# Kernel optimization log

Hardware: AMD Instinct MI355X
Metric: run time of the kernel (lower is better)

Reference implementation:

```python
import jax, jax.numpy as jnp
import numpy as np

HEADS = 12
EMBED = 768
HEAD_DIM = EMBED // HEADS


def setup_inputs() -> dict:
    key = jax.random.key(0)
    kx, kw, kb = jax.random.split(key, 3)
    x = jax.random.normal(kx, (8, 1024, EMBED), dtype=jnp.float32)
    # nn.Linear(embed, 3*embed): weight (3E, E), bias (3E,)
    W_qkv = jax.random.normal(kw, (3 * EMBED, EMBED), dtype=jnp.float32) * (1.0 / np.sqrt(EMBED))
    b_qkv = jax.random.normal(kb, (3 * EMBED,), dtype=jnp.float32) * 0.01
    return {"x": x, "W_qkv": W_qkv, "b_qkv": b_qkv}


def reference(x, W_qkv, b_qkv):
    b, n, e = x.shape
    qkv = x @ W_qkv.T + b_qkv                       # (b, n, 3E)
    qkv = qkv.reshape(b, n, HEADS, 3 * HEAD_DIM)    # (b, n, h, 3d)
    q, k, v = jnp.split(qkv, 3, axis=-1)            # each (b, n, h, d)
    scores = jnp.einsum('bihd,bjhd->bijh', q, k) / np.sqrt(HEAD_DIM)
    attn = jax.nn.softmax(scores, axis=-2)          # softmax over keys j (dim=-2)
    out = jnp.einsum('bijh,bjhd->bihd', attn, v)
    return out.reshape(b, n, e)
```

## Files before the change

kernel.cpp:

```cpp
#include <hip/hip_runtime.h>
#include <hip/hip_bf16.h>
#include <cstdint>
#include <math.h>

#define BATCH 8
#define SEQ   1024
#define EMB   768
#define HEADS 12
#define HDIM  64
#define C3    2304
#define MROWS (BATCH*SEQ)
#define NKT   (EMB / 32)
#define MTILES (MROWS / 128)
#define NTILES (C3 / 128)
#define XPACK_BLOCKS (MTILES * NKT)
#define WPACK_BLOCKS (NTILES * NKT)

typedef __attribute__((ext_vector_type(8)))  short bf16x8;
typedef __attribute__((ext_vector_type(4)))  short bf16x4;
typedef __attribute__((ext_vector_type(4)))  float f32x4;

static __device__ inline short f2bf(float f) {
    union { float f; uint32_t u; } v; v.f = f;
    uint32_t u = v.u + 0x7fff + ((v.u >> 16) & 1);
    return (short)(u >> 16);
}

static __device__ __forceinline__ void gload_lds16(const short* g, short* l) {
    __builtin_amdgcn_global_load_lds(
        (const __attribute__((address_space(1))) unsigned int*)g,
        (__attribute__((address_space(3))) unsigned int*)l, 16, 0, 0);
}

__global__ __launch_bounds__(256) void pack_bf16(const float* __restrict__ x,
                                                 short* __restrict__ xb2,
                                                 const float* __restrict__ W,
                                                 short* __restrict__ Wb2) {
    const float* in;
    short* out;
    int blk;
    if (blockIdx.x < XPACK_BLOCKS) {
        in = x; out = xb2; blk = blockIdx.x;
    } else {
        in = W; out = Wb2; blk = blockIdx.x - XPACK_BLOCKS;
    }
    const int mt = blk / NKT;
    const int kt = blk % NKT;
    short* obase = out + (size_t)blk * 4096;

    #pragma unroll
    for (int p = 0; p < 2; ++p) {
        int idx = p * 256 + threadIdx.x;
        int r = idx >> 2, s = idx & 3;
        const float* src = in + (size_t)(mt * 128 + r) * EMB + kt * 32 + s * 8;
        float4 v0 = ((const float4*)src)[0];
        float4 v1 = ((const float4*)src)[1];
        bf16x8 o = { f2bf(v0.x), f2bf(v0.y), f2bf(v0.z), f2bf(v0.w),
                     f2bf(v1.x), f2bf(v1.y), f2bf(v1.z), f2bf(v1.w) };
        int S = ((4 * r + s) ^ (r & 7));
        *(bf16x8*)(obase + S * 8) = o;
    }
}

#define LVP 136

__global__ __launch_bounds__(256) void qkv_gemm_mfma(const short* __restrict__ Apk,
                                                     const short* __restrict__ Bpk,
                                                     const float* __restrict__ bias,
                                                     short* __restrict__ qkvb,
                                                     short* __restrict__ vt) {
    __shared__ short smem[16384];
    short (*As)[4096] = (short (*)[4096])smem;
    short (*Bs)[4096] = (short (*)[4096])(smem + 8192);
    short* Lv = smem;

    const int g    = blockIdx.x;
    const int xcd  = g & 7;
    const int ring = g >> 3;
    const int by   = xcd * 8 + (ring & 7);
    const int bx   = ring >> 3;

    const int t    = threadIdx.x;
    const int w    = t >> 6;
    const int lane = t & 63;
    const int s4   = lane >> 4;
    const int r15  = lane & 15;
    const int m0 = by * 128, n0 = bx * 128;
    const int wm = (w & 1) * 64, wn = (w >> 1) * 64;

    const short* Ab = Apk + (size_t)by * (NKT * 4096);
    const short* Bb = Bpk + (size_t)bx * (NKT * 4096);

    int offA[4], offB[4];
    #pragma unroll
    for (int i = 0; i < 4; ++i) {
        int ra = wm + i * 16 + r15;
        offA[i] = ((4 * ra + s4) ^ (ra & 7)) << 3;
        int rb = wn + i * 16 + r15;
        offB[i] = ((4 * rb + s4) ^ (rb & 7)) << 3;
    }

    const int seg0 = w * 2;

#define STAGE(buf, kt) do {                                                   \
        const short* _a = Ab + (size_t)(kt) * 4096;                           \
        const short* _b = Bb + (size_t)(kt) * 4096;                           \
        gload_lds16(_a + (seg0    ) * 512 + lane * 8, &As[buf][(seg0    ) * 512]); \
        gload_lds16(_b + (seg0    ) * 512 + lane * 8, &Bs[buf][(seg0    ) * 512]); \
        gload_lds16(_a + (seg0 + 1) * 512 + lane * 8, &As[buf][(seg0 + 1) * 512]); \
        gload_lds16(_b + (seg0 + 1) * 512 + lane * 8, &Bs[buf][(seg0 + 1) * 512]); \
    } while (0)

    f32x4 acc[4][4] = {};

#define COMPUTE(buf) do {                                                     \
        bf16x8 af[4], bff[4];                                                 \
        _Pragma("unroll")                                                     \
        for (int i = 0; i < 4; ++i) {                                         \
            af[i]  = *(const bf16x8*)&As[buf][offA[i]];                       \
            bff[i] = *(const bf16x8*)&Bs[buf][offB[i]];                       \
        }                                                                     \
        _Pragma("unroll")                                                     \
        for (int mi = 0; mi < 4; ++mi)                                        \
            _Pragma("unroll")                                                 \
            for (int ni = 0; ni < 4; ++ni)                                    \
                acc[mi][ni] = __builtin_amdgcn_mfma_f32_16x16x32_bf16(        \
                    af[mi], bff[ni], acc[mi][ni], 0, 0, 0);                   \
    } while (0)

    STAGE(0, 0);
    __syncthreads();

    for (int kt = 0; kt < NKT; kt += 2) {
        STAGE(1, kt + 1);
        COMPUTE(0);
        __syncthreads();
        if (kt + 2 < NKT) STAGE(0, kt + 2);
        COMPUTE(1);
        __syncthreads();
    }
#undef STAGE
#undef COMPUTE

    const int bxm   = bx % 3;
    const bool has_v    = (bxm != 0);
    const int  wn_v     = (bxm == 1) ? 0 : 64;
    const bool is_vwave = has_v && (wn == wn_v);

    float bsv[4], scl[4];
    #pragma unroll
    for (int ni = 0; ni < 4; ++ni) {
        int n = n0 + wn + ni * 16 + r15;
        bsv[ni] = bias[n];
        scl[ni] = ((n % 192) < 64) ? 0.125f : 1.0f;
    }

    if (!is_vwave) {
        #pragma unroll
        for (int mi = 0; mi < 4; ++mi) {
            const int m = m0 + wm + mi * 16 + s4 * 4;
            #pragma unroll
            for (int ni = 0; ni < 4; ++ni) {
                const int n = n0 + wn + ni * 16 + r15;
                #pragma unroll
                for (int reg = 0; reg < 4; ++reg)
                    qkvb[(size_t)(m + reg) * C3 + n] =
                        f2bf((acc[mi][ni][reg] + bsv[ni]) * scl[ni]);
            }
        }
    } else {
        #pragma unroll
        for (int mi = 0; mi < 4; ++mi) {
            const int jl = wm + mi * 16 + s4 * 4;
            #pragma unroll
            for (int ni = 0; ni < 4; ++ni) {
                const int d = ni * 16 + r15;
                bf16x4 vv = { f2bf(acc[mi][ni][0] + bsv[ni]),
                              f2bf(acc[mi][ni][1] + bsv[ni]),
                              f2bf(acc[mi][ni][2] + bsv[ni]),
                              f2bf(acc[mi][ni][3] + bsv[ni]) };
                *(bf16x4*)&Lv[d * LVP + jl] = vv;
            }
        }
    }

    if (has_v) {
        __syncthreads();
        const int h  = (n0 + wn_v) / 192;
        const int bb = by >> 3;
        const int j0 = m0 & 1023;
        short* vrow = vt + ((size_t)(bb * HEADS + h) * 64) * SEQ + j0;
        #pragma unroll
        for (int p = 0; p < 4; ++p) {
            int lin = p * 256 + t;
            int d   = lin >> 4;
            int ch  = lin & 15;
            *(bf16x8*)(vrow + (size_t)d * SEQ + ch * 8) =
                *(bf16x8*)&Lv[d * LVP + ch * 8];
        }
    }
}

__global__ __launch_bounds__(256, 4) void attn_mfma(const short* __restrict__ qkvb,
                                                    const short* __restrict__ vt,
                                                    float* __restrict__ out) {
    __shared__ short Ks[64][64];
    __shared__ short Vt[64][64];
    __shared__ short Ps[64][64];

    const int g    = blockIdx.x;
    const int qt   = g / (BATCH * HEADS);
    const int bh   = g % (BATCH * HEADS);
    const int b    = bh / HEADS;
    const int h    = bh % HEADS;
    const int t    = threadIdx.x;
    const int w    = t >> 6;
    const int lane = t & 63;
    const int c    = lane & 15;
    const int q    = lane >> 4;
    const int ck   = c & 7;
    const int i0   = qt * 64;

    const size_t base = (size_t)b * SEQ * C3 + (size_t)h * 192;
    const short* vtb = vt + (size_t)bh * 64 * SEQ;
    const short* gk  = qkvb + base + 64;

    bf16x8 aq0, aq1;
    {
        const short* pq = qkvb + base + (size_t)(i0 + w * 16 + c) * C3 + q * 8;
        aq0 = *(const bf16x8*)(pq);
        aq1 = *(const bf16x8*)(pq + 32);
    }

    const int jA = t >> 3;
    const int jB = jA + 32;
    const int sg = t & 7;
    const int wKA = (sg ^ (jA & 7)) * 8;
    const int wKB = (sg ^ (jB & 7)) * 8;

    bf16x8 kr0, kr1, vr0, vr1;
    kr0 = *(const bf16x8*)(gk + (size_t)jA * C3 + sg * 8);
    kr1 = *(const bf16x8*)(gk + (size_t)jB * C3 + sg * 8);
    vr0 = *(const bf16x8*)(vtb + (size_t)jA * SEQ + sg * 8);
    vr1 = *(const bf16x8*)(vtb + (size_t)jB * SEQ + sg * 8);

    f32x4 o[4] = {};
    float l_acc = 0.f;

    for (int kt = 0; kt < 16; ++kt) {
        __syncthreads();
        *(bf16x8*)&Ks[jA][wKA] = kr0;
        *(bf16x8*)&Ks[jB][wKB] = kr1;
        *(bf16x8*)&Vt[jA][wKA] = vr0;
        *(bf16x8*)&Vt[jB][wKB] = vr1;
        __syncthreads();

        if (kt < 15) {
            const int j0 = (kt + 1) * 64;
            kr0 = *(const bf16x8*)(gk + (size_t)(j0 + jA) * C3 + sg * 8);
            kr1 = *(const bf16x8*)(gk + (size_t)(j0 + jB) * C3 + sg * 8);
            vr0 = *(const bf16x8*)(vtb + (size_t)jA * SEQ + j0 + sg * 8);
            vr1 = *(const bf16x8*)(vtb + (size_t)jB * SEQ + j0 + sg * 8);
        }

        bf16x8 ka[4][2];
        #pragma unroll
        for (int mt = 0; mt < 4; ++mt) {
            ka[mt][0] = *(bf16x8*)&Ks[mt * 16 + c][(q ^ ck) * 8];
            ka[mt][1] = *(bf16x8*)&Ks[mt * 16 + c][((4 + q) ^ ck) * 8];
        }

        f32x4 s[4];
        __builtin_amdgcn_s_setprio(1);
        #pragma unroll
        for (int mt = 0; mt < 4; ++mt) {
            f32x4 acc = {0.f, 0.f, 0.f, 0.f};
            acc = __builtin_amdgcn_mfma_f32_16x16x32_bf16(ka[mt][0], aq0, acc, 0, 0, 0);
            acc = __builtin_amdgcn_mfma_f32_16x16x32_bf16(ka[mt][1], aq1, acc, 0, 0, 0);
            s[mt] = acc;
        }
        __builtin_amdgcn_s_setprio(0);

        #pragma unroll
        for (int mt = 0; mt < 4; ++mt) {
            float p0 = __expf(s[mt][0]);
            float p1 = __expf(s[mt][1]);
            float p2 = __expf(s[mt][2]);
            float p3 = __expf(s[mt][3]);
            l_acc += (p0 + p1) + (p2 + p3);
            bf16x4 pw = { f2bf(p0), f2bf(p1), f2bf(p2), f2bf(p3) };
            int pcol = (((2 * mt + (q >> 1)) ^ ck) << 3) + (q & 1) * 4;
            *(bf16x4*)&Ps[w * 16 + c][pcol] = pw;
        }

        bf16x8 vb[4][2];
        #pragma unroll
        for (int dt = 0; dt < 4; ++dt) {
            vb[dt][0] = *(bf16x8*)&Vt[dt * 16 + c][(q ^ ck) * 8];
            vb[dt][1] = *(bf16x8*)&Vt[dt * 16 + c][((4 + q) ^ ck) * 8];
        }

        bf16x8 ap0 = *(bf16x8*)&Ps[w * 16 + c][(q ^ ck) * 8];
        bf16x8 ap1 = *(bf16x8*)&Ps[w * 16 + c][((4 + q) ^ ck) * 8];
        __builtin_amdgcn_s_setprio(1);
        #pragma unroll
        for (int dt = 0; dt < 4; ++dt) {
            o[dt] = __builtin_amdgcn_mfma_f32_16x16x32_bf16(ap0, vb[dt][0], o[dt], 0, 0, 0);
            o[dt] = __builtin_amdgcn_mfma_f32_16x16x32_bf16(ap1, vb[dt][1], o[dt], 0, 0, 0);
        }
        __builtin_amdgcn_s_setprio(0);
    }

    float v = l_acc;
    v += __shfl_xor(v, 16, 64);
    v += __shfl_xor(v, 32, 64);
    float linv[4];
    #pragma unroll
    for (int r = 0; r < 4; ++r)
        linv[r] = 1.0f / __shfl(v, 4 * q + r, 64);

    #pragma unroll
    for (int dt = 0; dt < 4; ++dt)
        #pragma unroll
        for (int r = 0; r < 4; ++r) {
            int i = w * 16 + q * 4 + r;
            out[((size_t)b * SEQ + i0 + i) * EMB + h * HDIM + dt * 16 + c]
                = o[dt][r] * linv[r];
        }
}

extern "C" void kernel_launch(void* const* d_in, const int* in_sizes, int n_in,
                              void* d_out, int out_size, void* d_ws, size_t ws_size,
                              hipStream_t stream) {
    const float* x    = (const float*)d_in[0];
    const float* W    = (const float*)d_in[1];
    const float* bias = (const float*)d_in[2];
    float* out = (float*)d_out;

    short* xb2  = (short*)d_ws;
    short* Wb2  = xb2 + (size_t)MROWS * EMB;
    short* qkvb = Wb2 + (size_t)C3 * EMB;
    short* vt   = qkvb + (size_t)MROWS * C3;

    pack_bf16<<<XPACK_BLOCKS + WPACK_BLOCKS, 256, 0, stream>>>(x, xb2, W, Wb2);

    qkv_gemm_mfma<<<1152, 256, 0, stream>>>(xb2, Wb2, bias, qkvb, vt);

    attn_mfma<<<BATCH * HEADS * (SEQ / 64), 256, 0, stream>>>(qkvb, vt, out);
}
```

Baseline: 172.1 us.

## Restructure QKV GEMM main loop with two-deep prefetch and fine-grained waitcnt barriers

Replaces the double-buffered loop, which used full __syncthreads after each compute, with a pipeline that keeps two k-tiles in flight. Each iteration reads fragments into registers, syncs, immediately reissues the global-to-LDS load into the freed buffer, then runs the MFMAs. Waits use explicit vmcnt/lgkmcnt counts so only the needed loads are awaited. MFMA blocks are wrapped in s_setprio to favor the matrix issue, at the cost of a more fragile hand-tuned schedule that relies on exact outstanding-load counts.

Result: faster. 160.7 us (-6.7%).

```diff
diff --git a/kernel.cpp b/kernel.cpp
--- a/kernel.cpp
+++ b/kernel.cpp
@@ -111,36 +111,61 @@
         gload_lds16(_b + (seg0 + 1) * 512 + lane * 8, &Bs[buf][(seg0 + 1) * 512]); \
     } while (0)
 
-    f32x4 acc[4][4] = {};
-
-#define COMPUTE(buf) do {                                                     \
-        bf16x8 af[4], bff[4];                                                 \
+#define LOAD_FRAGS(buf)                                                       \
         _Pragma("unroll")                                                     \
         for (int i = 0; i < 4; ++i) {                                         \
             af[i]  = *(const bf16x8*)&As[buf][offA[i]];                       \
             bff[i] = *(const bf16x8*)&Bs[buf][offB[i]];                       \
-        }                                                                     \
+        }
+
+#define MFMA16()                                                              \
+        __builtin_amdgcn_s_setprio(1);                                        \
         _Pragma("unroll")                                                     \
         for (int mi = 0; mi < 4; ++mi)                                        \
             _Pragma("unroll")                                                 \
             for (int ni = 0; ni < 4; ++ni)                                    \
                 acc[mi][ni] = __builtin_amdgcn_mfma_f32_16x16x32_bf16(        \
                     af[mi], bff[ni], acc[mi][ni], 0, 0, 0);                   \
-    } while (0)
+        __builtin_amdgcn_s_setprio(0);
+
+    f32x4 acc[4][4] = {};
+    bf16x8 af[4], bff[4];
 
     STAGE(0, 0);
-    __syncthreads();
-
-    for (int kt = 0; kt < NKT; kt += 2) {
-        STAGE(1, kt + 1);
-        COMPUTE(0);
-        __syncthreads();
-        if (kt + 2 < NKT) STAGE(0, kt + 2);
-        COMPUTE(1);
-        __syncthreads();
+    STAGE(1, 1);
+    asm volatile("s_waitcnt vmcnt(4)" ::: "memory");
+    __builtin_amdgcn_s_barrier();
+
+    for (int tt = 0; tt < NKT - 2; ++tt) {
+        const int buf = tt & 1;
+        LOAD_FRAGS(buf);
+        asm volatile("s_waitcnt lgkmcnt(0)" ::: "memory");
+        __builtin_amdgcn_sched_barrier(0);
+        __builtin_amdgcn_s_barrier();
+        STAGE(buf, tt + 2);
+        MFMA16();
+        asm volatile("s_waitcnt vmcnt(4)" ::: "memory");
+        __builtin_amdgcn_s_barrier();
+    }
+    {
+        LOAD_FRAGS((NKT - 2) & 1);
+        asm volatile("s_waitcnt lgkmcnt(0)" ::: "memory");
+        __builtin_amdgcn_sched_barrier(0);
+        __builtin_amdgcn_s_barrier();
+        MFMA16();
+        asm volatile("s_waitcnt vmcnt(0)" ::: "memory");
+        __builtin_amdgcn_s_barrier();
+    }
+    {
+        LOAD_FRAGS((NKT - 1) & 1);
+        asm volatile("s_waitcnt lgkmcnt(0)" ::: "memory");
+        __builtin_amdgcn_sched_barrier(0);
+        __builtin_amdgcn_s_barrier();
+        MFMA16();
     }
 #undef STAGE
-#undef COMPUTE
+#undef LOAD_FRAGS
+#undef MFMA16
 
     const int bxm   = bx % 3;
     const bool has_v    = (bxm != 0);
```
